# Kernel optimization log

Measured on AMD Instinct MI355X. Metric: run time of the kernel, lower is better.

Reference implementation:

```python
import jax, jax.numpy as jnp
import numpy as np

H = 16        # query heads
HK = 8        # key/value heads
HD = 128      # head dim
EPS = 1e-6
THETA = 1000000.0


def _rmsnorm(x, w):
    # per-head RMSNorm over last dim (head_dim)
    var = jnp.mean(jnp.square(x.astype(jnp.float32)), axis=-1, keepdims=True)
    return (x * jax.lax.rsqrt(var + EPS)).astype(x.dtype) * w


def _rope(x, cos, sin):
    # x: [B, S, h, HD]; cos/sin: [S, HD//2]
    x1, x2 = jnp.split(x, 2, axis=-1)
    c = cos[None, :, None, :]
    s = sin[None, :, None, :]
    return jnp.concatenate([x1 * c - x2 * s, x2 * c + x1 * s], axis=-1)


def setup_inputs() -> dict:
    key = jax.random.key(0)
    ks = jax.random.split(key, 5)
    B, S, D = 2, 2048, 2048
    scale = 0.02
    return {
        "x": jax.random.normal(ks[0], (B, S, D), jnp.float32),
        "wq": jax.random.normal(ks[1], (H * HD, D), jnp.float32) * scale,
        "wk": jax.random.normal(ks[2], (HK * HD, D), jnp.float32) * scale,
        "wv": jax.random.normal(ks[3], (HK * HD, D), jnp.float32) * scale,
        "wo": jax.random.normal(ks[4], (D, H * HD), jnp.float32) * scale,
        "q_norm_w": jnp.ones((HD,), jnp.float32),
        "k_norm_w": jnp.ones((HD,), jnp.float32),
    }


def reference(x, wq, wk, wv, wo, q_norm_w, k_norm_w):
    B, S, D = x.shape
    # QKV projections (no bias)
    q = (x @ wq.T).reshape(B, S, H, HD)
    k = (x @ wk.T).reshape(B, S, HK, HD)
    v = (x @ wv.T).reshape(B, S, HK, HD)

    # per-head RMSNorm on Q and K (Qwen3 qk-norm)
    q = _rmsnorm(q, q_norm_w)
    k = _rmsnorm(k, k_norm_w)

    # RoPE
    inv_freq = 1.0 / (THETA ** (jnp.arange(0, HD, 2, dtype=jnp.float32) / HD))
    ang = jnp.arange(S, dtype=jnp.float32)[:, None] * inv_freq[None, :]  # [S, HD/2]
    cos, sin = jnp.cos(ang), jnp.sin(ang)
    q = _rope(q, cos, sin)
    k = _rope(k, cos, sin)

    # GQA: repeat KV heads to match query heads
    rep = H // HK
    k = jnp.repeat(k, rep, axis=2)  # [B, S, H, HD]
    v = jnp.repeat(v, rep, axis=2)

    # causal SDPA
    scores = jnp.einsum("bqhd,bkhd->bhqk", q, k) / jnp.sqrt(jnp.float32(HD))
    mask = jnp.tril(jnp.ones((S, S), dtype=bool))
    scores = jnp.where(mask[None, None], scores, jnp.finfo(scores.dtype).min)
    probs = jax.nn.softmax(scores, axis=-1)
    out = jnp.einsum("bhqk,bkhd->bqhd", probs, v).reshape(B, S, H * HD)

    return out @ wo.T
```

## Files before the change

kernel.cpp:

```cpp
#include <hip/hip_runtime.h>
#include <hip/hip_bf16.h>
#include <math.h>

#define B_   2
#define S_   2048
#define D_   2048
#define H_   16
#define HK_  8
#define HD_  128
#define BS_  (B_ * S_)
#define NQKV 4096
#define SCALE 0.08838834764831845f

typedef __bf16 bf16x8 __attribute__((ext_vector_type(8)));
typedef __bf16 bf16x4 __attribute__((ext_vector_type(4)));
typedef float  f32x4  __attribute__((ext_vector_type(4)));

#define AS1(p) ((const __attribute__((address_space(1))) void*)(p))
#define AS3(p) ((__attribute__((address_space(3))) void*)(p))

template <int S>
__device__ __forceinline__ float ror16(float x) {
    return __builtin_bit_cast(float, __builtin_amdgcn_update_dpp(
        0, __builtin_bit_cast(int, x), 0x120 | S, 0xF, 0xF, true));
}
__device__ __forceinline__ float row_sum16(float x) {
    x += ror16<8>(x);
    x += ror16<4>(x);
    x += ror16<2>(x);
    x += ror16<1>(x);
    return x;
}

__global__ __launch_bounds__(256) void cvt_all(const float* __restrict__ x,
                                               const float* __restrict__ wq,
                                               const float* __restrict__ wk,
                                               const float* __restrict__ wv,
                                               const float* __restrict__ wo,
                                               __bf16* __restrict__ xb,
                                               __bf16* __restrict__ wb,
                                               __bf16* __restrict__ wob) {
    int bid = blockIdx.x;
    const float* src;
    __bf16* dst;
    int i4;
    if (bid < 8192)       { src = x;  dst = xb;                    i4 = bid * 256; }
    else if (bid < 12288) { src = wq; dst = wb;                    i4 = (bid - 8192) * 256; }
    else if (bid < 14336) { src = wk; dst = wb + (size_t)4194304;  i4 = (bid - 12288) * 256; }
    else if (bid < 16384) { src = wv; dst = wb + (size_t)6291456;  i4 = (bid - 14336) * 256; }
    else                  { src = wo; dst = wob;                   i4 = (bid - 16384) * 256; }
    i4 += threadIdx.x;
    float4 v = reinterpret_cast<const float4*>(src)[i4];
    bf16x4 o = {(__bf16)v.x, (__bf16)v.y, (__bf16)v.z, (__bf16)v.w};
    reinterpret_cast<bf16x4*>(dst)[i4] = o;
}

__global__ __launch_bounds__(128) void build_rope(float* __restrict__ tab) {
    int s = blockIdx.x;
    int d = threadIdx.x;
    int i = d & 63;
    float inv_freq = exp2f(-19.931568569324174f * (float)(2 * i) * (1.0f / 128.0f));
    float ang = (float)s * inv_freq;
    float sn, cs;
    sincosf(ang, &sn, &cs);
    tab[s * 128 + d] = (d < 64) ? cs : sn;
}

__global__ __launch_bounds__(512, 2) void gemm_bf16_8ph(const __bf16* __restrict__ A,
                                                        const __bf16* __restrict__ W,
                                                        __bf16* __restrict__ C,
                                                        int M, int N, int K) {
    __shared__ __bf16 lds[2][2][256 * 64];

    const int t    = threadIdx.x;
    const int w    = t >> 6;
    const int lane = t & 63;
    const int col  = lane & 15;
    const int quad = lane >> 4;
    const int c7   = col & 7;
    const int wm   = w >> 2;
    const int wn   = w & 3;

    const int bid = blockIdx.x;
    const int nid = (bid & 7) * 32 + (bid >> 3);
    const int st  = nid >> 4;
    const int wi  = nid & 15;
    const int m0 = ((st >> 2) * 4 + (wi >> 2)) * 256;
    const int n0 = ((st & 3) * 4 + (wi & 3)) * 256;

    const int lr8 = lane >> 3;
    const int sw8 = ((lane & 7) ^ lr8) * 8;
    const __bf16* Ag = A + (size_t)(m0 + w * 16 + lr8) * K + sw8;
    const __bf16* Wg = W + (size_t)(n0 + w * 16 + lr8) * K + sw8;

    const int nkt = K >> 6;
    const int nit = nkt >> 1;

    const int aBase = (wm * 128 + col) * 64;
    const int bBase = (wn * 64 + col) * 64;
    const int kx0 = (quad ^ c7) * 8;
    const int kx1 = ((4 + quad) ^ c7) * 8;

    f32x4 acc[8][4];
    #pragma unroll
    for (int i = 0; i < 8; i++)
        #pragma unroll
        for (int j = 0; j < 4; j++) acc[i][j] = (f32x4){0.f, 0.f, 0.f, 0.f};

    bf16x8 a[4][2], a2[4][2], b0f[2][2], b1f[2][2];

    auto stg = [&](int ktv, int bufc, int ab, int half) {
        if (ktv >= nkt) return;
        const __bf16* gb = (ab ? Wg : Ag) + (size_t)half * 128 * K + (size_t)ktv * 64;
        __bf16* db = &lds[bufc][ab][(half * 128 + w * 16) * 64];
        __builtin_amdgcn_global_load_lds(AS1(gb), AS3(db), 16, 0, 0);
        __builtin_amdgcn_global_load_lds(AS1(gb + (size_t)8 * K), AS3(db + 512), 16, 0, 0);
    };
    auto lda = [&](bf16x8 (&dst)[4][2], const __bf16* panel, int g) {
        #pragma unroll
        for (int mi = 0; mi < 4; mi++) {
            dst[mi][0] = *reinterpret_cast<const bf16x8*>(&panel[aBase + (g * 64 + mi * 16) * 64 + kx0]);
            dst[mi][1] = *reinterpret_cast<const bf16x8*>(&panel[aBase + (g * 64 + mi * 16) * 64 + kx1]);
        }
    };
    auto ldb = [&](bf16x8 (&dst)[2][2], const __bf16* panel, int ng) {
        #pragma unroll
        for (int ni = 0; ni < 2; ni++) {
            dst[ni][0] = *reinterpret_cast<const bf16x8*>(&panel[bBase + (ng * 32 + ni * 16) * 64 + kx0]);
            dst[ni][1] = *reinterpret_cast<const bf16x8*>(&panel[bBase + (ng * 32 + ni * 16) * 64 + kx1]);
        }
    };
    auto mm = [&](bf16x8 (&af)[4][2], bf16x8 (&bfr)[2][2], int g, int ng) {
        __builtin_amdgcn_s_setprio(1);
        #pragma unroll
        for (int mi = 0; mi < 4; mi++)
            #pragma unroll
            for (int ni = 0; ni < 2; ni++) {
                f32x4 c = acc[g * 4 + mi][ng * 2 + ni];
                c = __builtin_amdgcn_mfma_f32_16x16x32_bf16(af[mi][0], bfr[ni][0], c, 0, 0, 0);
                c = __builtin_amdgcn_mfma_f32_16x16x32_bf16(af[mi][1], bfr[ni][1], c, 0, 0, 0);
                acc[g * 4 + mi][ng * 2 + ni] = c;
            }
        __builtin_amdgcn_s_setprio(0);
    };

#define BAR  __builtin_amdgcn_s_barrier()
#define LGKM0 do { asm volatile("s_waitcnt lgkmcnt(0)" ::: "memory"); \
                   __builtin_amdgcn_sched_barrier(0); } while (0)
#define VM(n) asm volatile("s_waitcnt vmcnt(" #n ")" ::: "memory")

    stg(0, 0, 0, 0); stg(0, 0, 0, 1); stg(0, 0, 1, 0); stg(0, 0, 1, 1);
    stg(1, 1, 0, 0); stg(1, 1, 0, 1);
    VM(4);
    BAR;

    #pragma unroll 1
    for (int it = 0; it < nit; ++it) {
        const int k2 = it * 2;
        const bool last = (it == nit - 1);

        const __bf16* A0p = &lds[0][0][0];
        const __bf16* B0p = &lds[0][1][0];
        const __bf16* A1p = &lds[1][0][0];
        const __bf16* B1p = &lds[1][1][0];

        lda(a, A0p, 0); ldb(b0f, B0p, 0);
        stg(k2 + 1, 1, 1, 0);
        BAR; LGKM0;
        mm(a, b0f, 0, 0);
        lda(a2, A0p, 1);
        stg(k2 + 1, 1, 1, 1);
        BAR; LGKM0;
        mm(a2, b0f, 1, 0);
        ldb(b1f, B0p, 1);
        stg(k2 + 2, 0, 0, 0);
        BAR; LGKM0;
        mm(a, b1f, 0, 1);
        stg(k2 + 2, 0, 0, 1);
        if (last) VM(0); else VM(4);
        BAR;
        mm(a2, b1f, 1, 1);

        lda(a, A1p, 0); ldb(b0f, B1p, 0);
        stg(k2 + 2, 0, 1, 0);
        BAR; LGKM0;
        mm(a, b0f, 0, 0);
        lda(a2, A1p, 1);
        stg(k2 + 2, 0, 1, 1);
        BAR; LGKM0;
        mm(a2, b0f, 1, 0);
        ldb(b1f, B1p, 1);
        stg(k2 + 3, 1, 0, 0);
        BAR; LGKM0;
        mm(a, b1f, 0, 1);
        stg(k2 + 3, 1, 0, 1);
        if (!last) { VM(4); }
        BAR;
        mm(a2, b1f, 1, 1);
    }

#undef BAR
#undef LGKM0
#undef VM

    #pragma unroll
    for (int m8 = 0; m8 < 8; m8++) {
        #pragma unroll
        for (int r = 0; r < 4; r++) {
            size_t row = m0 + wm * 128 + m8 * 16 + quad * 4 + r;
            __bf16* cp = C + row * N + n0 + wn * 64 + col;
            #pragma unroll
            for (int n4 = 0; n4 < 4; n4++) cp[n4 * 16] = (__bf16)acc[m8][n4][r];
        }
    }
}

template <typename CT>
__global__ __launch_bounds__(256) void gemm_bf16_nt_n64(const __bf16* __restrict__ A,
                                                        const __bf16* __restrict__ W,
                                                        CT* __restrict__ C,
                                                        int M, int N, int K) {
    __shared__ __bf16 As[128 * 64];
    __shared__ __bf16 Bs[64 * 64];

    const int t    = threadIdx.x;
    const int w    = t >> 6;
    const int lane = t & 63;
    const int col  = lane & 15;
    const int quad = lane >> 4;
    const int wm   = w >> 1;
    const int wn   = w & 1;

    const int m0 = blockIdx.x * 128;
    const int n0 = blockIdx.y * 64;

    const int lrow8 = lane >> 3;
    const int lch   = ((lane & 7) ^ lrow8) * 8;

    const __bf16* agp = A + (size_t)(m0 + w * 32 + lrow8) * K + lch;
    const __bf16* wgp = W + (size_t)(n0 + w * 16 + lrow8) * K + lch;
    __bf16* alp = As + (w * 32) * 64;
    __bf16* blp = Bs + (w * 16) * 64;

    const int c7 = col & 7;

    f32x4 acc[4][2];
    #pragma unroll
    for (int m = 0; m < 4; m++)
        #pragma unroll
        for (int n = 0; n < 2; n++) acc[m][n] = (f32x4){0.f, 0.f, 0.f, 0.f};

    #pragma unroll 1
    for (int k0 = 0; k0 < K; k0 += 64) {
        #pragma unroll
        for (int j = 0; j < 4; j++)
            __builtin_amdgcn_global_load_lds(AS1(agp + k0 + (size_t)(j * 8) * K),
                                             AS3(alp + j * 512), 16, 0, 0);
        #pragma unroll
        for (int j = 0; j < 2; j++)
            __builtin_amdgcn_global_load_lds(AS1(wgp + k0 + (size_t)(j * 8) * K),
                                             AS3(blp + j * 512), 16, 0, 0);
        __syncthreads();

        #pragma unroll
        for (int kk = 0; kk < 2; kk++) {
            bf16x8 af[4], bfr[2];
            #pragma unroll
            for (int m = 0; m < 4; m++)
                af[m] = *reinterpret_cast<const bf16x8*>(
                    &As[(wm * 64 + m * 16 + col) * 64 + ((kk * 4 + quad) ^ c7) * 8]);
            #pragma unroll
            for (int n = 0; n < 2; n++)
                bfr[n] = *reinterpret_cast<const bf16x8*>(
                    &Bs[(wn * 32 + n * 16 + col) * 64 + ((kk * 4 + quad) ^ c7) * 8]);

            #pragma unroll
            for (int m = 0; m < 4; m++)
                #pragma unroll
                for (int n = 0; n < 2; n++)
                    acc[m][n] = __builtin_amdgcn_mfma_f32_16x16x32_bf16(af[m], bfr[n], acc[m][n], 0, 0, 0);
        }
        __syncthreads();
    }

    #pragma unroll
    for (int m = 0; m < 4; m++) {
        #pragma unroll
        for (int r = 0; r < 4; r++) {
            size_t row = m0 + wm * 64 + m * 16 + quad * 4 + r;
            CT* cp = C + row * N + n0 + wn * 32 + col;
            #pragma unroll
            for (int n = 0; n < 2; n++) cp[n * 16] = (CT)acc[m][n][r];
        }
    }
}

__global__ __launch_bounds__(256) void norm_rope(__bf16* __restrict__ qkv,
                                                 const float* __restrict__ qw,
                                                 const float* __restrict__ kw,
                                                 const float* __restrict__ tab) {
    const int g    = blockIdx.x * 16 + (threadIdx.x >> 4);
    const int l    = threadIdx.x & 15;
    const int row  = g / 24;
    const int head = g - row * 24;
    const int s    = row & (S_ - 1);

    const float* w = (head < H_) ? qw : kw;
    __bf16* p = qkv + (size_t)row * NQKV + head * HD_ + l * 8;

    bf16x8 xv = *reinterpret_cast<const bf16x8*>(p);
    float xf[8];
    float ss = 0.f;
    #pragma unroll
    for (int j = 0; j < 8; j++) { xf[j] = (float)xv[j]; ss = fmaf(xf[j], xf[j], ss); }
    ss = row_sum16(ss);
    float rs = rsqrtf(ss * (1.0f / 128.0f) + 1e-6f);

    float nf[8];
    const float4 w0 = *reinterpret_cast<const float4*>(&w[l * 8]);
    const float4 w1 = *reinterpret_cast<const float4*>(&w[l * 8 + 4]);
    nf[0] = xf[0] * rs * w0.x; nf[1] = xf[1] * rs * w0.y;
    nf[2] = xf[2] * rs * w0.z; nf[3] = xf[3] * rs * w0.w;
    nf[4] = xf[4] * rs * w1.x; nf[5] = xf[5] * rs * w1.y;
    nf[6] = xf[6] * rs * w1.z; nf[7] = xf[7] * rs * w1.w;

    float of[8];
    #pragma unroll
    for (int j = 0; j < 8; j++) of[j] = __shfl_xor(nf[j], 8);

    const int ib = (l & 7) * 8;
    const float4 c0 = *reinterpret_cast<const float4*>(&tab[s * 128 + ib]);
    const float4 c1 = *reinterpret_cast<const float4*>(&tab[s * 128 + ib + 4]);
    const float4 s0 = *reinterpret_cast<const float4*>(&tab[s * 128 + 64 + ib]);
    const float4 s1 = *reinterpret_cast<const float4*>(&tab[s * 128 + 64 + ib + 4]);
    float cs[8] = {c0.x, c0.y, c0.z, c0.w, c1.x, c1.y, c1.z, c1.w};
    float sn[8] = {s0.x, s0.y, s0.z, s0.w, s1.x, s1.y, s1.z, s1.w};

    bf16x8 out;
    if (l < 8) {
        #pragma unroll
        for (int j = 0; j < 8; j++) out[j] = (__bf16)(nf[j] * cs[j] - of[j] * sn[j]);
    } else {
        #pragma unroll
        for (int j = 0; j < 8; j++) out[j] = (__bf16)(of[j] * sn[j] + nf[j] * cs[j]);
    }
    *reinterpret_cast<bf16x8*>(p) = out;
}

__global__ __launch_bounds__(256) void transpose_v(const __bf16* __restrict__ qkv,
                                                   __bf16* __restrict__ vt) {
    __shared__ __bf16 Ls[64][136];
    const int t  = threadIdx.x;
    const int bk = blockIdx.y;
    const int b  = bk >> 3;
    const int kvh = bk & 7;
    const int s0 = blockIdx.x * 64;

    #pragma unroll
    for (int i = 0; i < 4; i++) {
        int f = t + i * 256;
        int row = f >> 4;
        int d8 = (f & 15) * 8;
        bf16x8 v = *reinterpret_cast<const bf16x8*>(
            &qkv[(size_t)(b * S_ + s0 + row) * NQKV + 3072 + kvh * HD_ + d8]);
        *reinterpret_cast<bf16x8*>(&Ls[row][d8]) = v;
    }
    __syncthreads();

    #pragma unroll
    for (int i = 0; i < 4; i++) {
        int f = t + i * 256;
        int dim = f >> 3;
        int kc = f & 7;
        bf16x8 o;
        #pragma unroll
        for (int e = 0; e < 8; e++) o[e] = Ls[kc * 8 + e][dim];
        *reinterpret_cast<bf16x8*>(
            &vt[((size_t)bk * HD_ + dim) * S_ + s0 + kc * 8]) = o;
    }
}

__global__ __launch_bounds__(256) void attn_mfma(const __bf16* __restrict__ qkv,
                                                 const __bf16* __restrict__ vt,
                                                 __bf16* __restrict__ ao) {
    __shared__ __align__(16) char smem[17408];
    __bf16 (*Qs)[136] = reinterpret_cast<__bf16(*)[136]>(smem);
    __bf16 (*Ks)[136] = reinterpret_cast<__bf16(*)[136]>(smem);
    __shared__ __bf16 Vt[128][72];
    __shared__ __bf16 Ps[4][16][72];

    const int t    = threadIdx.x;
    const int w    = t >> 6;
    const int lane = t & 63;
    const int col  = lane & 15;
    const int quad = lane >> 4;

    const int bh  = blockIdx.x;
    const int b   = bh >> 4;
    const int h   = bh & 15;
    const int kvh = h >> 1;
    const int qb  = gridDim.y - 1 - blockIdx.y;
    const int r0  = qb * 64;

    const float C0 = SCALE * 1.44269504f;
    const float CM = -12.0f * 1.44269504f;

    const __bf16* vbase = vt + ((size_t)(b * HK_ + kvh) * HD_) * S_;

    const __bf16* kp[4];
    __bf16*       kw_[4];
    const __bf16* vp[4];
    __bf16*       vw_[4];
    #pragma unroll
    for (int i = 0; i < 4; i++) {
        int f = t + i * 256;
        int row = f >> 4, d8 = (f & 15) * 8;
        kp[i]  = qkv + (size_t)(b * S_ + row) * NQKV + 2048 + kvh * HD_ + d8;
        kw_[i] = &Ks[row][d8];
        int dim = f >> 3, kc = f & 7;
        vp[i]  = vbase + (size_t)dim * S_ + kc * 8;
        vw_[i] = &Vt[dim][kc * 8];
    }

    bf16x8 kreg[4], vreg[4];
    #pragma unroll
    for (int i = 0; i < 4; i++) {
        kreg[i] = *reinterpret_cast<const bf16x8*>(kp[i]);  kp[i] += (size_t)64 * NQKV;
        vreg[i] = *reinterpret_cast<const bf16x8*>(vp[i]);  vp[i] += 64;
    }

    #pragma unroll
    for (int i = 0; i < 4; i++) {
        int f   = t + i * 256;
        int row = f >> 4;
        int d8  = (f & 15) * 8;
        bf16x8 v = *reinterpret_cast<const bf16x8*>(
            &qkv[(size_t)(b * S_ + r0 + row) * NQKV + h * HD_ + d8]);
        *reinterpret_cast<bf16x8*>(&Qs[row][d8]) = v;
    }
    __syncthreads();

    bf16x8 qf[4];
    {
        const int m = w * 16 + col;
        #pragma unroll
        for (int k = 0; k < 4; k++)
            qf[k] = *reinterpret_cast<const bf16x8*>(&Qs[m][k * 32 + quad * 8]);
    }

    f32x4 o_acc[8];
    #pragma unroll
    for (int i = 0; i < 8; i++) o_acc[i] = (f32x4){0.f, 0.f, 0.f, 0.f};
    float l_lane[4] = {0.f, 0.f, 0.f, 0.f};

    const int ntiles = qb + 1;
    for (int ti = 0; ti < ntiles; ti++) {
        __syncthreads();

        #pragma unroll
        for (int i = 0; i < 4; i++) {
            *reinterpret_cast<bf16x8*>(kw_[i]) = kreg[i];
            *reinterpret_cast<bf16x8*>(vw_[i]) = vreg[i];
        }
        if (ti + 1 < ntiles) {
            #pragma unroll
            for (int i = 0; i < 4; i++) {
                kreg[i] = *reinterpret_cast<const bf16x8*>(kp[i]);  kp[i] += (size_t)64 * NQKV;
                vreg[i] = *reinterpret_cast<const bf16x8*>(vp[i]);  vp[i] += 64;
            }
        }
        __syncthreads();

        f32x4 s[4];
        #pragma unroll
        for (int n = 0; n < 4; n++) {
            f32x4 acc = (f32x4){0.f, 0.f, 0.f, 0.f};
            #pragma unroll
            for (int k = 0; k < 4; k++) {
                bf16x8 bf = *reinterpret_cast<const bf16x8*>(
                    &Ks[n * 16 + col][k * 32 + quad * 8]);
                acc = __builtin_amdgcn_mfma_f32_16x16x32_bf16(qf[k], bf, acc, 0, 0, 0);
            }
            s[n] = acc;
        }

        const bool diag = (ti == qb);
        #pragma unroll
        for (int r = 0; r < 4; r++) {
            float p0 = exp2f(fmaf(s[0][r], C0, CM));
            float p1 = exp2f(fmaf(s[1][r], C0, CM));
            float p2 = exp2f(fmaf(s[2][r], C0, CM));
            float p3 = exp2f(fmaf(s[3][r], C0, CM));
            if (diag) {
                int qloc = w * 16 + quad * 4 + r;
                if (0 * 16 + col > qloc) p0 = 0.f;
                if (1 * 16 + col > qloc) p1 = 0.f;
                if (2 * 16 + col > qloc) p2 = 0.f;
                if (3 * 16 + col > qloc) p3 = 0.f;
            }
            l_lane[r] += p0 + p1 + p2 + p3;
            Ps[w][quad * 4 + r][0 * 16 + col] = (__bf16)p0;
            Ps[w][quad * 4 + r][1 * 16 + col] = (__bf16)p1;
            Ps[w][quad * 4 + r][2 * 16 + col] = (__bf16)p2;
            Ps[w][quad * 4 + r][3 * 16 + col] = (__bf16)p3;
        }

        bf16x8 pf[2];
        #pragma unroll
        for (int ks = 0; ks < 2; ks++)
            pf[ks] = *reinterpret_cast<const bf16x8*>(&Ps[w][col][ks * 32 + quad * 8]);
        #pragma unroll
        for (int n = 0; n < 8; n++) {
            #pragma unroll
            for (int ks = 0; ks < 2; ks++) {
                bf16x8 vf = *reinterpret_cast<const bf16x8*>(
                    &Vt[n * 16 + col][ks * 32 + quad * 8]);
                o_acc[n] = __builtin_amdgcn_mfma_f32_16x16x32_bf16(pf[ks], vf, o_acc[n], 0, 0, 0);
            }
        }
    }

    #pragma unroll
    for (int r = 0; r < 4; r++) {
        float l = row_sum16(l_lane[r]);
        float inv = 1.0f / l;
        int qrow = r0 + w * 16 + quad * 4 + r;
        __bf16* op = ao + (size_t)(b * S_ + qrow) * (H_ * HD_) + h * HD_ + col;
        #pragma unroll
        for (int n = 0; n < 8; n++)
            op[n * 16] = (__bf16)(o_acc[n][r] * inv);
    }
}

extern "C" void kernel_launch(void* const* d_in, const int* in_sizes, int n_in,
                              void* d_out, int out_size, void* d_ws, size_t ws_size,
                              hipStream_t stream) {
    const float* x  = (const float*)d_in[0];
    const float* wq = (const float*)d_in[1];
    const float* wk = (const float*)d_in[2];
    const float* wv = (const float*)d_in[3];
    const float* wo = (const float*)d_in[4];
    const float* qw = (const float*)d_in[5];
    const float* kw = (const float*)d_in[6];
    float* out = (float*)d_out;

    __bf16* ws  = (__bf16*)d_ws;
    __bf16* xb  = ws;
    __bf16* wb  = xb  + (size_t)8388608;
    __bf16* wob = wb  + (size_t)8388608;
    __bf16* qkv = wob + (size_t)4194304;
    __bf16* ao  = qkv + (size_t)16777216;
    __bf16* vtg = ao  + (size_t)8388608;
    float* rtab = (float*)ao;

    cvt_all<<<20480, 256, 0, stream>>>(x, wq, wk, wv, wo, xb, wb, wob);
    build_rope<<<S_, 128, 0, stream>>>(rtab);

    gemm_bf16_8ph<<<256, 512, 0, stream>>>(xb, wb, qkv, BS_, NQKV, D_);

    norm_rope<<<(BS_ * 24) / 16, 256, 0, stream>>>(qkv, qw, kw, rtab);

    transpose_v<<<dim3(S_ / 64, B_ * HK_), 256, 0, stream>>>(qkv, vtg);

    attn_mfma<<<dim3(B_ * H_, S_ / 64), 256, 0, stream>>>(qkv, vtg, ao);

    gemm_bf16_nt_n64<float><<<dim3(BS_ / 128, D_ / 64), 256, 0, stream>>>(
        ao, wob, out, BS_, D_, H_ * HD_);
}
```

Baseline: 333.1 us.

## Restructure GEMM main loop to one barrier per k-tile with partial lgkm waits

Rewrites the double-buffered k-loop of the 256x128 bf16 GEMM so each k-tile synchronises with a single barrier instead of four. It relies on partial lgkmcnt waits so MFMAs start while later LDS fragment reads are still in flight, and it preloads the next tile's first fragments right after the barrier. The aim is to cut barrier stalls and expose more overlap between LDS reads and MFMA. In exchange, the whole next tile is staged at once and waited on with vmcnt(0), so global-load prefetch depth drops and latency may be exposed. It also uses an extra fragment register set, which raises register pressure.

```diff
diff --git a/kernel.cpp b/kernel.cpp
--- a/kernel.cpp
+++ b/kernel.cpp
@@ -107,7 +107,7 @@
         #pragma unroll
         for (int j = 0; j < 4; j++) acc[i][j] = (f32x4){0.f, 0.f, 0.f, 0.f};
 
-    bf16x8 a[4][2], a2[4][2], b0f[2][2], b1f[2][2];
+    bf16x8 aE[4][2], aO[4][2], a2[4][2], b0f[2][2], b1f[2][2];
 
     auto stg = [&](int ktv, int bufc, int ab, int half) {
         if (ktv >= nkt) return;
@@ -145,62 +145,60 @@
     };
 
 #define BAR  __builtin_amdgcn_s_barrier()
-#define LGKM0 do { asm volatile("s_waitcnt lgkmcnt(0)" ::: "memory"); \
-                   __builtin_amdgcn_sched_barrier(0); } while (0)
+#define LGKM(n) do { asm volatile("s_waitcnt lgkmcnt(" #n ")" ::: "memory"); \
+                     __builtin_amdgcn_sched_barrier(0); } while (0)
 #define VM(n) asm volatile("s_waitcnt vmcnt(" #n ")" ::: "memory")
 
+    const __bf16* P0a = &lds[0][0][0];
+    const __bf16* P0b = &lds[0][1][0];
+    const __bf16* P1a = &lds[1][0][0];
+    const __bf16* P1b = &lds[1][1][0];
+
     stg(0, 0, 0, 0); stg(0, 0, 0, 1); stg(0, 0, 1, 0); stg(0, 0, 1, 1);
-    stg(1, 1, 0, 0); stg(1, 1, 0, 1);
-    VM(4);
+    VM(0);
     BAR;
+    lda(aE, P0a, 0); ldb(b0f, P0b, 0);
 
     #pragma unroll 1
     for (int it = 0; it < nit; ++it) {
-        const int k2 = it * 2;
-        const bool last = (it == nit - 1);
-
-        const __bf16* A0p = &lds[0][0][0];
-        const __bf16* B0p = &lds[0][1][0];
-        const __bf16* A1p = &lds[1][0][0];
-        const __bf16* B1p = &lds[1][1][0];
-
-        lda(a, A0p, 0); ldb(b0f, B0p, 0);
-        stg(k2 + 1, 1, 1, 0);
-        BAR; LGKM0;
-        mm(a, b0f, 0, 0);
-        lda(a2, A0p, 1);
-        stg(k2 + 1, 1, 1, 1);
-        BAR; LGKM0;
+        const int T0 = it * 2;
+        const int T1 = T0 + 1;
+
+        lda(a2, P0a, 1);
+        stg(T1, 1, 0, 0); stg(T1, 1, 0, 1);
+        LGKM(8);
+        mm(aE, b0f, 0, 0);
+        ldb(b1f, P0b, 1);
+        stg(T1, 1, 1, 0); stg(T1, 1, 1, 1);
+        LGKM(4);
         mm(a2, b0f, 1, 0);
-        ldb(b1f, B0p, 1);
-        stg(k2 + 2, 0, 0, 0);
-        BAR; LGKM0;
-        mm(a, b1f, 0, 1);
-        stg(k2 + 2, 0, 0, 1);
-        if (last) VM(0); else VM(4);
+        LGKM(0);
+        mm(a2, b1f, 1, 1);
+        mm(aE, b1f, 0, 1);
+        VM(0);
         BAR;
+        lda(aO, P1a, 0); ldb(b0f, P1b, 0);
+
+        lda(a2, P1a, 1);
+        stg(T1 + 1, 0, 0, 0); stg(T1 + 1, 0, 0, 1);
+        LGKM(8);
+        mm(aO, b0f, 0, 0);
+        ldb(b1f, P1b, 1);
+        stg(T1 + 1, 0, 1, 0); stg(T1 + 1, 0, 1, 1);
+        LGKM(4);
+        mm(a2, b0f, 1, 0);
+        LGKM(0);
         mm(a2, b1f, 1, 1);
-
-        lda(a, A1p, 0); ldb(b0f, B1p, 0);
-        stg(k2 + 2, 0, 1, 0);
-        BAR; LGKM0;
-        mm(a, b0f, 0, 0);
-        lda(a2, A1p, 1);
-        stg(k2 + 2, 0, 1, 1);
-        BAR; LGKM0;
-        mm(a2, b0f, 1, 0);
-        ldb(b1f, B1p, 1);
-        stg(k2 + 3, 1, 0, 0);
-        BAR; LGKM0;
-        mm(a, b1f, 0, 1);
-        stg(k2 + 3, 1, 0, 1);
-        if (!last) { VM(4); }
-        BAR;
-        mm(a2, b1f, 1, 1);
+        mm(aO, b1f, 0, 1);
+        if (it + 1 < nit) {
+            VM(0);
+            BAR;
+            lda(aE, P0a, 0); ldb(b0f, P0b, 0);
+        }
     }
 
 #undef BAR
-#undef LGKM0
+#undef LGKM
 #undef VM
 
     #pragma unroll
```

Measured after the change: 406.3 us. +22.0%, slower.

## Double attention query tile to 128 rows with 512-thread blocks

Applied to the files above, without the earlier changes.

The attention kernel now processes 128 query rows per block using 8 waves instead of 64 rows with 4 waves. Each K/V tile staged in shared memory is reused by twice as many queries, halving global K/V traffic per query. The Q fragments are loaded straight from global memory instead of going through shared memory. The causal mask logic is adjusted for two diagonal tiles per block. The trade-offs are half as many blocks (less parallelism and coarser causal load balance) and wasted work on the upper diagonal tile.

```diff
diff --git a/kernel.cpp b/kernel.cpp
--- a/kernel.cpp
+++ b/kernel.cpp
@@ -380,14 +380,12 @@
     }
 }
 
-__global__ __launch_bounds__(256) void attn_mfma(const __bf16* __restrict__ qkv,
-                                                 const __bf16* __restrict__ vt,
-                                                 __bf16* __restrict__ ao) {
-    __shared__ __align__(16) char smem[17408];
-    __bf16 (*Qs)[136] = reinterpret_cast<__bf16(*)[136]>(smem);
-    __bf16 (*Ks)[136] = reinterpret_cast<__bf16(*)[136]>(smem);
+__global__ __launch_bounds__(512, 4) void attn_mfma(const __bf16* __restrict__ qkv,
+                                                    const __bf16* __restrict__ vt,
+                                                    __bf16* __restrict__ ao) {
+    __shared__ __bf16 Ks[64][136];
     __shared__ __bf16 Vt[128][72];
-    __shared__ __bf16 Ps[4][16][72];
+    __shared__ __bf16 Ps[8][16][72];
 
     const int t    = threadIdx.x;
     const int w    = t >> 6;
@@ -400,20 +398,20 @@
     const int h   = bh & 15;
     const int kvh = h >> 1;
     const int qb  = gridDim.y - 1 - blockIdx.y;
-    const int r0  = qb * 64;
+    const int r0  = qb * 128;
 
     const float C0 = SCALE * 1.44269504f;
     const float CM = -12.0f * 1.44269504f;
 
     const __bf16* vbase = vt + ((size_t)(b * HK_ + kvh) * HD_) * S_;
 
-    const __bf16* kp[4];
-    __bf16*       kw_[4];
-    const __bf16* vp[4];
-    __bf16*       vw_[4];
-    #pragma unroll
-    for (int i = 0; i < 4; i++) {
-        int f = t + i * 256;
+    const __bf16* kp[2];
+    __bf16*       kw_[2];
+    const __bf16* vp[2];
+    __bf16*       vw_[2];
+    #pragma unroll
+    for (int i = 0; i < 2; i++) {
+        int f = t + i * 512;
         int row = f >> 4, d8 = (f & 15) * 8;
         kp[i]  = qkv + (size_t)(b * S_ + row) * NQKV + 2048 + kvh * HD_ + d8;
         kw_[i] = &Ks[row][d8];
@@ -422,54 +420,45 @@
         vw_[i] = &Vt[dim][kc * 8];
     }
 
-    bf16x8 kreg[4], vreg[4];
-    #pragma unroll
-    for (int i = 0; i < 4; i++) {
+    bf16x8 kreg[2], vreg[2];
+    #pragma unroll
+    for (int i = 0; i < 2; i++) {
         kreg[i] = *reinterpret_cast<const bf16x8*>(kp[i]);  kp[i] += (size_t)64 * NQKV;
         vreg[i] = *reinterpret_cast<const bf16x8*>(vp[i]);  vp[i] += 64;
     }
 
-    #pragma unroll
-    for (int i = 0; i < 4; i++) {
-        int f   = t + i * 256;
-        int row = f >> 4;
-        int d8  = (f & 15) * 8;
-        bf16x8 v = *reinterpret_cast<const bf16x8*>(
-            &qkv[(size_t)(b * S_ + r0 + row) * NQKV + h * HD_ + d8]);
-        *reinterpret_cast<bf16x8*>(&Qs[row][d8]) = v;
-    }
-    __syncthreads();
-
     bf16x8 qf[4];
-    {
-        const int m = w * 16 + col;
-        #pragma unroll
-        for (int k = 0; k < 4; k++)
-            qf[k] = *reinterpret_cast<const bf16x8*>(&Qs[m][k * 32 + quad * 8]);
-    }
+    #pragma unroll
+    for (int k = 0; k < 4; k++)
+        qf[k] = *reinterpret_cast<const bf16x8*>(
+            &qkv[(size_t)(b * S_ + r0 + w * 16 + col) * NQKV
+                 + h * HD_ + k * 32 + quad * 8]);
 
     f32x4 o_acc[8];
     #pragma unroll
     for (int i = 0; i < 8; i++) o_acc[i] = (f32x4){0.f, 0.f, 0.f, 0.f};
     float l_lane[4] = {0.f, 0.f, 0.f, 0.f};
 
-    const int ntiles = qb + 1;
+    const int ntiles = 2 * qb + 2;
     for (int ti = 0; ti < ntiles; ti++) {
         __syncthreads();
 
         #pragma unroll
-        for (int i = 0; i < 4; i++) {
+        for (int i = 0; i < 2; i++) {
             *reinterpret_cast<bf16x8*>(kw_[i]) = kreg[i];
             *reinterpret_cast<bf16x8*>(vw_[i]) = vreg[i];
         }
         if (ti + 1 < ntiles) {
             #pragma unroll
-            for (int i = 0; i < 4; i++) {
+            for (int i = 0; i < 2; i++) {
                 kreg[i] = *reinterpret_cast<const bf16x8*>(kp[i]);  kp[i] += (size_t)64 * NQKV;
                 vreg[i] = *reinterpret_cast<const bf16x8*>(vp[i]);  vp[i] += 64;
             }
         }
         __syncthreads();
+
+        const bool diag = (ti >= 2 * qb);
+        const int toff = (ti - 2 * qb) * 64;
 
         f32x4 s[4];
         #pragma unroll
@@ -484,7 +473,6 @@
             s[n] = acc;
         }
 
-        const bool diag = (ti == qb);
         #pragma unroll
         for (int r = 0; r < 4; r++) {
             float p0 = exp2f(fmaf(s[0][r], C0, CM));
@@ -492,11 +480,11 @@
             float p2 = exp2f(fmaf(s[2][r], C0, CM));
             float p3 = exp2f(fmaf(s[3][r], C0, CM));
             if (diag) {
-                int qloc = w * 16 + quad * 4 + r;
-                if (0 * 16 + col > qloc) p0 = 0.f;
-                if (1 * 16 + col > qloc) p1 = 0.f;
-                if (2 * 16 + col > qloc) p2 = 0.f;
-                if (3 * 16 + col > qloc) p3 = 0.f;
+                int qrel = w * 16 + quad * 4 + r;
+                if (toff + 0 * 16 + col > qrel) p0 = 0.f;
+                if (toff + 1 * 16 + col > qrel) p1 = 0.f;
+                if (toff + 2 * 16 + col > qrel) p2 = 0.f;
+                if (toff + 3 * 16 + col > qrel) p3 = 0.f;
             }
             l_lane[r] += p0 + p1 + p2 + p3;
             Ps[w][quad * 4 + r][0 * 16 + col] = (__bf16)p0;
@@ -562,7 +550,7 @@
 
     transpose_v<<<dim3(S_ / 64, B_ * HK_), 256, 0, stream>>>(qkv, vtg);
 
-    attn_mfma<<<dim3(B_ * H_, S_ / 64), 256, 0, stream>>>(qkv, vtg, ao);
+    attn_mfma<<<dim3(B_ * H_, S_ / 128), 512, 0, stream>>>(qkv, vtg, ao);
 
     gemm_bf16_nt_n64<float><<<dim3(BS_ / 128, D_ / 64), 256, 0, stream>>>(
         ao, wob, out, BS_, D_, H_ * HD_);
```

After: 346.9 us. 1.04x slower.
